# Kernel optimization log

Hardware: AMD Instinct MI355X
Metric: run time of the kernel (lower is better)

The kernel has to match this reference:

```python
import jax, jax.numpy as jnp
import numpy as np

VOCAB = 50000
D = 256          # vector_dim == hidden size
SEQ = 128
BATCH = 4096
NUM_CLASSES = 5


def setup_inputs() -> dict:
    key = jax.random.key(0)
    ks = jax.random.split(key, 8)
    x = jax.random.randint(ks[0], (BATCH, SEQ), 0, VOCAB, dtype=jnp.int64)
    scale = 1.0 / np.sqrt(D)
    emb = jax.random.normal(ks[1], (VOCAB, D), dtype=jnp.float32)
    emb = emb.at[0].set(0.0)  # padding_idx=0 row is zero
    W_ih = jax.random.uniform(ks[2], (D, D), jnp.float32, -scale, scale)
    W_hh = jax.random.uniform(ks[3], (D, D), jnp.float32, -scale, scale)
    b_ih = jax.random.uniform(ks[4], (D,), jnp.float32, -scale, scale)
    b_hh = jax.random.uniform(ks[5], (D,), jnp.float32, -scale, scale)
    W_cls = jax.random.uniform(ks[6], (NUM_CLASSES, D), jnp.float32, -scale, scale)
    b_cls = jax.random.uniform(ks[7], (NUM_CLASSES,), jnp.float32, -scale, scale)
    return {"x": x, "emb": emb, "W_ih": W_ih, "W_hh": W_hh,
            "b_ih": b_ih, "b_hh": b_hh, "W_cls": W_cls, "b_cls": b_cls}


def reference(x, emb, W_ih, W_hh, b_ih, b_hh, W_cls, b_cls):
    # Embedding lookup: [B, S, D]
    xe = emb[x]
    # Precompute input projections for all timesteps in one GEMM.
    x_proj = jnp.einsum("bsd,hd->bsh", xe, W_ih) + b_ih + b_hh  # [B, S, D]

    def step(h, xp_t):
        h = jnp.tanh(xp_t + h @ W_hh.T)
        return h, None

    h0 = jnp.zeros((x.shape[0], W_hh.shape[0]), dtype=xe.dtype)
    # scan over time axis: [S, B, D]
    h_last, _ = jax.lax.scan(step, h0, jnp.swapaxes(x_proj, 0, 1))
    # classifier on last step
    return h_last @ W_cls.T + b_cls  # [B, 5]
```

## Files before the change

kernel.cpp:

```cpp
#include <hip/hip_runtime.h>


typedef __attribute__((ext_vector_type(8))) short bf16x8;
typedef __attribute__((ext_vector_type(4))) float f32x4;

#define VOCAB 50000
#define NBLK_EMB 256
#define LDS_STRIDE 264

__device__ __align__(256) unsigned short g_P[VOCAB * 256];

static __device__ __forceinline__ float bf2f(unsigned short u) {
    union { unsigned int i; float f; } v; v.i = ((unsigned int)u) << 16; return v.f;
}
static __device__ __forceinline__ float bfbits2f(unsigned int zext_u16) {
    union { unsigned int i; float f; } v; v.i = zext_u16 << 16; return v.f;
}
static __device__ __forceinline__ unsigned short f2bf_rne(float f) {
    union { float f; unsigned int i; } v; v.f = f;
    unsigned int r = v.i + 0x7FFFu + ((v.i >> 16) & 1u);
    return (unsigned short)(r >> 16);
}
static __device__ __forceinline__ unsigned short f2bf_fast(float f) {
    union { float f; unsigned int i; } v; v.f = f;
    return (unsigned short)((v.i + 0x8000u) >> 16);
}
static __device__ __forceinline__ bf16x8 cvt8(float4 a, float4 b) {
    bf16x8 r;
    r[0] = (short)f2bf_rne(a.x); r[1] = (short)f2bf_rne(a.y);
    r[2] = (short)f2bf_rne(a.z); r[3] = (short)f2bf_rne(a.w);
    r[4] = (short)f2bf_rne(b.x); r[5] = (short)f2bf_rne(b.y);
    r[6] = (short)f2bf_rne(b.z); r[7] = (short)f2bf_rne(b.w);
    return r;
}
static __device__ __forceinline__ bf16x8 load8_bf(const float* __restrict__ p) {
    return cvt8(((const float4*)p)[0], ((const float4*)p)[1]);
}
static __device__ __forceinline__ float fast_tanh(float x) {
    x = __builtin_amdgcn_fmed3f(x, -8.f, 8.f);
    float e = __expf(2.f * x);
    return __builtin_fmaf(-2.f, __builtin_amdgcn_rcpf(e + 1.f), 1.f);
}

__global__ __launch_bounds__(256)
void emb_proj_kernel(const float* __restrict__ emb,
                     const float* __restrict__ W_ih,
                     const float* __restrict__ b_ih,
                     const float* __restrict__ b_hh)
{
    __shared__ __align__(16) unsigned short tin [16 * LDS_STRIDE];
    __shared__ __align__(16) unsigned short tout[16 * LDS_STRIDE];
    const int tid  = threadIdx.x;
    const int lane = tid & 63;
    const int wid  = tid >> 6;
    const int n0   = wid * 64;
    const int row  = tid >> 4, seg = tid & 15;

    bf16x8 wf[4][8];
    float  bias[4];
    #pragma unroll
    for (int nt = 0; nt < 4; ++nt) {
        int n = n0 + nt * 16 + (lane & 15);
        bias[nt] = b_ih[n] + b_hh[n];
        #pragma unroll
        for (int kt = 0; kt < 8; ++kt)
            wf[nt][kt] = load8_bf(W_ih + n * 256 + (lane >> 4) * 8 + kt * 32);
    }

    int tile = blockIdx.x;
    float4 a0, a1, a2, a3;
    {
        const float4* s = (const float4*)(emb + ((size_t)tile * 16 + row) * 256 + seg * 16);
        a0 = s[0]; a1 = s[1]; a2 = s[2]; a3 = s[3];
    }

    for (; tile < 3125; tile += NBLK_EMB) {
        *(bf16x8*)(&tin[row * LDS_STRIDE + seg * 16])     = cvt8(a0, a1);
        *(bf16x8*)(&tin[row * LDS_STRIDE + seg * 16 + 8]) = cvt8(a2, a3);
        int tn = tile + NBLK_EMB;
        if (tn < 3125) {
            const float4* s = (const float4*)(emb + ((size_t)tn * 16 + row) * 256 + seg * 16);
            a0 = s[0]; a1 = s[1]; a2 = s[2]; a3 = s[3];
        }
        __syncthreads();

        f32x4 acc[4];
        #pragma unroll
        for (int nt = 0; nt < 4; ++nt) acc[nt] = (f32x4){0.f, 0.f, 0.f, 0.f};
        #pragma unroll
        for (int kt = 0; kt < 8; ++kt) {
            bf16x8 a = *(bf16x8*)(&tin[(lane & 15) * LDS_STRIDE + (lane >> 4) * 8 + kt * 32]);
            #pragma unroll
            for (int nt = 0; nt < 4; ++nt)
                acc[nt] = __builtin_amdgcn_mfma_f32_16x16x32_bf16(a, wf[nt][kt], acc[nt], 0, 0, 0);
        }
        #pragma unroll
        for (int nt = 0; nt < 4; ++nt) {
            int n = n0 + nt * 16 + (lane & 15);
            #pragma unroll
            for (int r = 0; r < 4; ++r)
                tout[((lane >> 4) * 4 + r) * LDS_STRIDE + n] = f2bf_rne(acc[nt][r] + bias[nt]);
        }
        __syncthreads();
        {
            uint4 o0 = *(uint4*)(&tout[row * LDS_STRIDE + seg * 16]);
            uint4 o1 = *(uint4*)(&tout[row * LDS_STRIDE + seg * 16 + 8]);
            uint4* dst = (uint4*)(g_P + ((size_t)tile * 16 + row) * 256 + seg * 16);
            dst[0] = o0; dst[1] = o1;
        }
    }
}

__global__ __launch_bounds__(512, 2)
void rnn_kernel(const int* __restrict__ x,
                const float* __restrict__ W_hh,
                const float* __restrict__ W_cls,
                const float* __restrict__ b_cls,
                float* __restrict__ out)
{
    __shared__ __align__(16) unsigned short h_lds[2][16 * 256];
    __shared__ __align__(16) int tok_t[128 * 16];
    __shared__ __align__(16) float wcls_lds[5 * 256];
    __shared__ float bcls_lds[5];

    const int tid  = threadIdx.x;
    const int lane = tid & 63;
    const int wid  = tid >> 6;
    const int b0   = blockIdx.x * 16;
    const int n0   = wid * 32;
    const int l15  = lane & 15;
    const int quad = lane >> 4;

    bf16x8 wf[2][8];
    #pragma unroll
    for (int nt = 0; nt < 2; ++nt) {
        int n = n0 + nt * 16 + l15;
        #pragma unroll
        for (int kt = 0; kt < 8; ++kt)
            wf[nt][kt] = load8_bf(W_hh + n * 256 + quad * 8 + kt * 32);
    }

    {
        int row = tid & 15, tq = tid >> 4;
        int4 v = *(const int4*)(x + (size_t)(b0 + row) * 128 + tq * 4);
        tok_t[(tq * 4 + 0) * 16 + row] = v.x;
        tok_t[(tq * 4 + 1) * 16 + row] = v.y;
        tok_t[(tq * 4 + 2) * 16 + row] = v.z;
        tok_t[(tq * 4 + 3) * 16 + row] = v.w;
    }
    if (tid < 320) ((float4*)wcls_lds)[tid] = ((const float4*)W_cls)[tid];
    if (tid < 5)   bcls_lds[tid] = b_cls[tid];
    #pragma unroll
    for (int i = 0; i < 4; ++i) ((unsigned int*)h_lds[0])[tid + i * 512] = 0;

    int aoff[8];
    #pragma unroll
    for (int kt = 0; kt < 8; ++kt)
        aoff[kt] = l15 * 512 + (((quad + 4 * kt) ^ l15) << 4);
    int woff[8];
    #pragma unroll
    for (int nt = 0; nt < 2; ++nt)
        #pragma unroll
        for (int r = 0; r < 4; ++r) {
            int row = quad * 4 + r;
            int g   = (n0 >> 3) + nt * 2 + (l15 >> 3);
            woff[nt * 4 + r] = row * 512 + ((g ^ row) << 4) + (l15 & 7) * 2;
        }

    const unsigned int colByte = (unsigned int)(n0 + l15) * 2;

    unsigned int gA[8], gB[8];
    #pragma unroll
    for (int r = 0; r < 4; ++r) {
        const int* xr = x + (size_t)(b0 + quad * 4 + r) * 128;
        const unsigned short* p0 = g_P + (size_t)xr[0] * 256 + n0 + l15;
        const unsigned short* p1 = g_P + (size_t)xr[1] * 256 + n0 + l15;
        gA[r] = p0[0]; gA[4 + r] = p0[16];
        gB[r] = p1[0]; gB[4 + r] = p1[16];
    }
    __syncthreads();

    char* const h0 = (char*)&h_lds[0][0];

    auto step = [&](const char* hA, char* hW, unsigned int* g, int t) {
        f32x4 acc0 = { bfbits2f(g[0]), bfbits2f(g[1]), bfbits2f(g[2]), bfbits2f(g[3]) };
        f32x4 acc1 = { bfbits2f(g[4]), bfbits2f(g[5]), bfbits2f(g[6]), bfbits2f(g[7]) };
        if (t + 2 < 128) {
            int4 tk = *(const int4*)&tok_t[(t + 2) * 16 + quad * 4];
            const unsigned short* r0 = (const unsigned short*)((const char*)g_P + ((unsigned int)tk.x * 512 + colByte));
            const unsigned short* r1 = (const unsigned short*)((const char*)g_P + ((unsigned int)tk.y * 512 + colByte));
            const unsigned short* r2 = (const unsigned short*)((const char*)g_P + ((unsigned int)tk.z * 512 + colByte));
            const unsigned short* r3 = (const unsigned short*)((const char*)g_P + ((unsigned int)tk.w * 512 + colByte));
            g[0] = r0[0]; g[4] = r0[16];
            g[1] = r1[0]; g[5] = r1[16];
            g[2] = r2[0]; g[6] = r2[16];
            g[3] = r3[0]; g[7] = r3[16];
        }
        #pragma unroll
        for (int kt = 0; kt < 8; ++kt) {
            bf16x8 a = *(const bf16x8*)(hA + aoff[kt]);
            acc0 = __builtin_amdgcn_mfma_f32_16x16x32_bf16(a, wf[0][kt], acc0, 0, 0, 0);
            acc1 = __builtin_amdgcn_mfma_f32_16x16x32_bf16(a, wf[1][kt], acc1, 0, 0, 0);
        }
        #pragma unroll
        for (int r = 0; r < 4; ++r) {
            *(unsigned short*)(hW + woff[r])     = f2bf_fast(fast_tanh(acc0[r]));
            *(unsigned short*)(hW + woff[4 + r]) = f2bf_fast(fast_tanh(acc1[r]));
        }
    };

    #pragma unroll 1
    for (int t2 = 0; t2 < 64; ++t2) {
        step(h0,        h0 + 8192, gA, 2 * t2);
        __syncthreads();
        step(h0 + 8192, h0,        gB, 2 * t2 + 1);
        __syncthreads();
    }

    if (tid < 320) {
        int q = tid & 3, p = tid >> 2;
        int row = p / 5, c = p - row * 5;
        float acc = 0.f;
        #pragma unroll
        for (int kk = 0; kk < 64; ++kk) {
            int k = q * 64 + kk;
            int off = row * 512 + ((((k >> 3) ^ row)) << 4) + (k & 7) * 2;
            acc += bf2f(*(const unsigned short*)(h0 + off)) * wcls_lds[c * 256 + k];
        }
        acc += __shfl_xor(acc, 1);
        acc += __shfl_xor(acc, 2);
        if (q == 0) out[(size_t)(b0 + row) * 5 + c] = acc + bcls_lds[c];
    }
}

extern "C" void kernel_launch(void* const* d_in, const int* in_sizes, int n_in,
                              void* d_out, int out_size, void* d_ws, size_t ws_size,
                              hipStream_t stream)
{
    const int*   x     = (const int*)d_in[0];
    const float* emb   = (const float*)d_in[1];
    const float* W_ih  = (const float*)d_in[2];
    const float* W_hh  = (const float*)d_in[3];
    const float* b_ih  = (const float*)d_in[4];
    const float* b_hh  = (const float*)d_in[5];
    const float* W_cls = (const float*)d_in[6];
    const float* b_cls = (const float*)d_in[7];
    float*       out   = (float*)d_out;
    (void)d_ws; (void)ws_size;

    emb_proj_kernel<<<NBLK_EMB, 256, 0, stream>>>(emb, W_ih, b_ih, b_hh);
    rnn_kernel<<<256, 512, 0, stream>>>(x, W_hh, W_cls, b_cls, out);
}
```

Baseline: 229.6 us.

## Drop LDS staging in embedding projection and use LDS-only barriers in RNN loop

The embedding projection kernel now loads each wave's A fragments straight from global memory into registers and writes results straight to the global table. This removes the LDS staging buffers and both block barriers per tile, and the grid size and occupancy hint are doubled. In the recurrent kernel, __syncthreads is replaced with a barrier that waits only on LDS/scalar counters, so in-flight global gathers of the next step's projections no longer stall each step's barrier. The risks are uncoalesced 2-byte global stores, redundant A loads across the four waves, and relying on the custom barrier being a correct memory fence for the h_lds exchange.

```diff
diff --git a/kernel.cpp b/kernel.cpp
--- a/kernel.cpp
+++ b/kernel.cpp
@@ -5,8 +5,7 @@
 typedef __attribute__((ext_vector_type(4))) float f32x4;
 
 #define VOCAB 50000
-#define NBLK_EMB 256
-#define LDS_STRIDE 264
+#define NBLK_EMB 512
 
 __device__ __align__(256) unsigned short g_P[VOCAB * 256];
 
@@ -41,72 +40,57 @@
     float e = __expf(2.f * x);
     return __builtin_fmaf(-2.f, __builtin_amdgcn_rcpf(e + 1.f), 1.f);
 }
-
-__global__ __launch_bounds__(256)
+static __device__ __forceinline__ void barrier_lds_only() {
+    asm volatile("s_waitcnt lgkmcnt(0)\n\ts_barrier" ::: "memory");
+}
+
+__global__ __launch_bounds__(256, 2)
 void emb_proj_kernel(const float* __restrict__ emb,
                      const float* __restrict__ W_ih,
                      const float* __restrict__ b_ih,
                      const float* __restrict__ b_hh)
 {
-    __shared__ __align__(16) unsigned short tin [16 * LDS_STRIDE];
-    __shared__ __align__(16) unsigned short tout[16 * LDS_STRIDE];
     const int tid  = threadIdx.x;
     const int lane = tid & 63;
     const int wid  = tid >> 6;
     const int n0   = wid * 64;
-    const int row  = tid >> 4, seg = tid & 15;
+    const int l15  = lane & 15;
+    const int quad = lane >> 4;
 
     bf16x8 wf[4][8];
     float  bias[4];
     #pragma unroll
     for (int nt = 0; nt < 4; ++nt) {
-        int n = n0 + nt * 16 + (lane & 15);
+        int n = n0 + nt * 16 + l15;
         bias[nt] = b_ih[n] + b_hh[n];
         #pragma unroll
         for (int kt = 0; kt < 8; ++kt)
-            wf[nt][kt] = load8_bf(W_ih + n * 256 + (lane >> 4) * 8 + kt * 32);
-    }
-
-    int tile = blockIdx.x;
-    float4 a0, a1, a2, a3;
-    {
-        const float4* s = (const float4*)(emb + ((size_t)tile * 16 + row) * 256 + seg * 16);
-        a0 = s[0]; a1 = s[1]; a2 = s[2]; a3 = s[3];
-    }
-
-    for (; tile < 3125; tile += NBLK_EMB) {
-        *(bf16x8*)(&tin[row * LDS_STRIDE + seg * 16])     = cvt8(a0, a1);
-        *(bf16x8*)(&tin[row * LDS_STRIDE + seg * 16 + 8]) = cvt8(a2, a3);
-        int tn = tile + NBLK_EMB;
-        if (tn < 3125) {
-            const float4* s = (const float4*)(emb + ((size_t)tn * 16 + row) * 256 + seg * 16);
-            a0 = s[0]; a1 = s[1]; a2 = s[2]; a3 = s[3];
-        }
-        __syncthreads();
+            wf[nt][kt] = load8_bf(W_ih + n * 256 + quad * 8 + kt * 32);
+    }
+
+    for (int tile = blockIdx.x; tile < 3125; tile += NBLK_EMB) {
+        const float* arow = emb + ((size_t)tile * 16 + l15) * 256 + quad * 8;
+        bf16x8 a[8];
+        #pragma unroll
+        for (int kt = 0; kt < 8; ++kt)
+            a[kt] = load8_bf(arow + kt * 32);
 
         f32x4 acc[4];
         #pragma unroll
         for (int nt = 0; nt < 4; ++nt) acc[nt] = (f32x4){0.f, 0.f, 0.f, 0.f};
         #pragma unroll
         for (int kt = 0; kt < 8; ++kt) {
-            bf16x8 a = *(bf16x8*)(&tin[(lane & 15) * LDS_STRIDE + (lane >> 4) * 8 + kt * 32]);
             #pragma unroll
             for (int nt = 0; nt < 4; ++nt)
-                acc[nt] = __builtin_amdgcn_mfma_f32_16x16x32_bf16(a, wf[nt][kt], acc[nt], 0, 0, 0);
-        }
+                acc[nt] = __builtin_amdgcn_mfma_f32_16x16x32_bf16(a[kt], wf[nt][kt], acc[nt], 0, 0, 0);
+        }
+
+        unsigned short* prow = g_P + ((size_t)tile * 16 + quad * 4) * 256 + n0;
         #pragma unroll
         for (int nt = 0; nt < 4; ++nt) {
-            int n = n0 + nt * 16 + (lane & 15);
             #pragma unroll
             for (int r = 0; r < 4; ++r)
-                tout[((lane >> 4) * 4 + r) * LDS_STRIDE + n] = f2bf_rne(acc[nt][r] + bias[nt]);
-        }
-        __syncthreads();
-        {
-            uint4 o0 = *(uint4*)(&tout[row * LDS_STRIDE + seg * 16]);
-            uint4 o1 = *(uint4*)(&tout[row * LDS_STRIDE + seg * 16 + 8]);
-            uint4* dst = (uint4*)(g_P + ((size_t)tile * 16 + row) * 256 + seg * 16);
-            dst[0] = o0; dst[1] = o1;
+                prow[r * 256 + nt * 16 + l15] = f2bf_rne(acc[nt][r] + bias[nt]);
         }
     }
 }
@@ -178,7 +162,7 @@
         gA[r] = p0[0]; gA[4 + r] = p0[16];
         gB[r] = p1[0]; gB[4 + r] = p1[16];
     }
-    __syncthreads();
+    barrier_lds_only();
 
     char* const h0 = (char*)&h_lds[0][0];
 
@@ -212,9 +196,9 @@
     #pragma unroll 1
     for (int t2 = 0; t2 < 64; ++t2) {
         step(h0,        h0 + 8192, gA, 2 * t2);
-        __syncthreads();
+        barrier_lds_only();
         step(h0 + 8192, h0,        gB, 2 * t2 + 1);
-        __syncthreads();
+        barrier_lds_only();
     }
 
     if (tid < 320) {
```

Result: slower. 258.8 us (+12.7%).

## Halve RNN block to 4 waves with 64 columns each; lighter barriers

Applied to the files above, without the earlier changes.

The recurrent kernel now runs 256 threads per block, and each wave owns 64 hidden columns (four MFMA N-tiles) instead of 32. This halves the number of waves that meet at each per-timestep barrier and gives each wave more independent MFMAs, at the cost of more registers per wave and fewer waves per CU. Barriers are replaced by a raw s_waitcnt lgkmcnt(0) + s_barrier, so outstanding global gathers no longer stall the barrier. The embedding-projection kernel also gets twice as many blocks and a 2-blocks-per-CU launch bound.

```diff
diff --git a/kernel.cpp b/kernel.cpp
--- a/kernel.cpp
+++ b/kernel.cpp
@@ -5,7 +5,7 @@
 typedef __attribute__((ext_vector_type(4))) float f32x4;
 
 #define VOCAB 50000
-#define NBLK_EMB 256
+#define NBLK_EMB 512
 #define LDS_STRIDE 264
 
 __device__ __align__(256) unsigned short g_P[VOCAB * 256];
@@ -41,8 +41,11 @@
     float e = __expf(2.f * x);
     return __builtin_fmaf(-2.f, __builtin_amdgcn_rcpf(e + 1.f), 1.f);
 }
-
-__global__ __launch_bounds__(256)
+static __device__ __forceinline__ void barrier_lds_only() {
+    asm volatile("s_waitcnt lgkmcnt(0)\n\ts_barrier" ::: "memory");
+}
+
+__global__ __launch_bounds__(256, 2)
 void emb_proj_kernel(const float* __restrict__ emb,
                      const float* __restrict__ W_ih,
                      const float* __restrict__ b_ih,
@@ -82,7 +85,7 @@
             const float4* s = (const float4*)(emb + ((size_t)tn * 16 + row) * 256 + seg * 16);
             a0 = s[0]; a1 = s[1]; a2 = s[2]; a3 = s[3];
         }
-        __syncthreads();
+        barrier_lds_only();
 
         f32x4 acc[4];
         #pragma unroll
@@ -101,7 +104,7 @@
             for (int r = 0; r < 4; ++r)
                 tout[((lane >> 4) * 4 + r) * LDS_STRIDE + n] = f2bf_rne(acc[nt][r] + bias[nt]);
         }
-        __syncthreads();
+        barrier_lds_only();
         {
             uint4 o0 = *(uint4*)(&tout[row * LDS_STRIDE + seg * 16]);
             uint4 o1 = *(uint4*)(&tout[row * LDS_STRIDE + seg * 16 + 8]);
@@ -111,7 +114,7 @@
     }
 }
 
-__global__ __launch_bounds__(512, 2)
+__global__ __launch_bounds__(256, 1)
 void rnn_kernel(const int* __restrict__ x,
                 const float* __restrict__ W_hh,
                 const float* __restrict__ W_cls,
@@ -127,13 +130,13 @@
     const int lane = tid & 63;
     const int wid  = tid >> 6;
     const int b0   = blockIdx.x * 16;
-    const int n0   = wid * 32;
+    const int n0   = wid * 64;
     const int l15  = lane & 15;
     const int quad = lane >> 4;
 
-    bf16x8 wf[2][8];
-    #pragma unroll
-    for (int nt = 0; nt < 2; ++nt) {
+    bf16x8 wf[4][8];
+    #pragma unroll
+    for (int nt = 0; nt < 4; ++nt) {
         int n = n0 + nt * 16 + l15;
         #pragma unroll
         for (int kt = 0; kt < 8; ++kt)
@@ -142,24 +145,29 @@
 
     {
         int row = tid & 15, tq = tid >> 4;
-        int4 v = *(const int4*)(x + (size_t)(b0 + row) * 128 + tq * 4);
-        tok_t[(tq * 4 + 0) * 16 + row] = v.x;
-        tok_t[(tq * 4 + 1) * 16 + row] = v.y;
-        tok_t[(tq * 4 + 2) * 16 + row] = v.z;
-        tok_t[(tq * 4 + 3) * 16 + row] = v.w;
-    }
-    if (tid < 320) ((float4*)wcls_lds)[tid] = ((const float4*)W_cls)[tid];
-    if (tid < 5)   bcls_lds[tid] = b_cls[tid];
-    #pragma unroll
-    for (int i = 0; i < 4; ++i) ((unsigned int*)h_lds[0])[tid + i * 512] = 0;
+        int4 v0 = *(const int4*)(x + (size_t)(b0 + row) * 128 + tq * 8);
+        int4 v1 = *(const int4*)(x + (size_t)(b0 + row) * 128 + tq * 8 + 4);
+        tok_t[(tq * 8 + 0) * 16 + row] = v0.x;
+        tok_t[(tq * 8 + 1) * 16 + row] = v0.y;
+        tok_t[(tq * 8 + 2) * 16 + row] = v0.z;
+        tok_t[(tq * 8 + 3) * 16 + row] = v0.w;
+        tok_t[(tq * 8 + 4) * 16 + row] = v1.x;
+        tok_t[(tq * 8 + 5) * 16 + row] = v1.y;
+        tok_t[(tq * 8 + 6) * 16 + row] = v1.z;
+        tok_t[(tq * 8 + 7) * 16 + row] = v1.w;
+    }
+    for (int i = tid; i < 320; i += 256) ((float4*)wcls_lds)[i] = ((const float4*)W_cls)[i];
+    if (tid < 5) bcls_lds[tid] = b_cls[tid];
+    #pragma unroll
+    for (int i = 0; i < 8; ++i) ((unsigned int*)h_lds[0])[tid + i * 256] = 0;
 
     int aoff[8];
     #pragma unroll
     for (int kt = 0; kt < 8; ++kt)
         aoff[kt] = l15 * 512 + (((quad + 4 * kt) ^ l15) << 4);
-    int woff[8];
-    #pragma unroll
-    for (int nt = 0; nt < 2; ++nt)
+    int woff[16];
+    #pragma unroll
+    for (int nt = 0; nt < 4; ++nt)
         #pragma unroll
         for (int r = 0; r < 4; ++r) {
             int row = quad * 4 + r;
@@ -169,66 +177,75 @@
 
     const unsigned int colByte = (unsigned int)(n0 + l15) * 2;
 
-    unsigned int gA[8], gB[8];
+    unsigned int gA[16], gB[16];
     #pragma unroll
     for (int r = 0; r < 4; ++r) {
         const int* xr = x + (size_t)(b0 + quad * 4 + r) * 128;
         const unsigned short* p0 = g_P + (size_t)xr[0] * 256 + n0 + l15;
         const unsigned short* p1 = g_P + (size_t)xr[1] * 256 + n0 + l15;
-        gA[r] = p0[0]; gA[4 + r] = p0[16];
-        gB[r] = p1[0]; gB[4 + r] = p1[16];
-    }
-    __syncthreads();
+        #pragma unroll
+        for (int nt = 0; nt < 4; ++nt) {
+            gA[nt * 4 + r] = p0[nt * 16];
+            gB[nt * 4 + r] = p1[nt * 16];
+        }
+    }
+    barrier_lds_only();
 
     char* const h0 = (char*)&h_lds[0][0];
 
     auto step = [&](const char* hA, char* hW, unsigned int* g, int t) {
-        f32x4 acc0 = { bfbits2f(g[0]), bfbits2f(g[1]), bfbits2f(g[2]), bfbits2f(g[3]) };
-        f32x4 acc1 = { bfbits2f(g[4]), bfbits2f(g[5]), bfbits2f(g[6]), bfbits2f(g[7]) };
+        f32x4 acc[4];
+        #pragma unroll
+        for (int nt = 0; nt < 4; ++nt)
+            acc[nt] = (f32x4){ bfbits2f(g[nt*4+0]), bfbits2f(g[nt*4+1]),
+                               bfbits2f(g[nt*4+2]), bfbits2f(g[nt*4+3]) };
         if (t + 2 < 128) {
             int4 tk = *(const int4*)&tok_t[(t + 2) * 16 + quad * 4];
-            const unsigned short* r0 = (const unsigned short*)((const char*)g_P + ((unsigned int)tk.x * 512 + colByte));
-            const unsigned short* r1 = (const unsigned short*)((const char*)g_P + ((unsigned int)tk.y * 512 + colByte));
-            const unsigned short* r2 = (const unsigned short*)((const char*)g_P + ((unsigned int)tk.z * 512 + colByte));
-            const unsigned short* r3 = (const unsigned short*)((const char*)g_P + ((unsigned int)tk.w * 512 + colByte));
-            g[0] = r0[0]; g[4] = r0[16];
-            g[1] = r1[0]; g[5] = r1[16];
-            g[2] = r2[0]; g[6] = r2[16];
-            g[3] = r3[0]; g[7] = r3[16];
+            const char* r0 = (const char*)g_P + ((unsigned int)tk.x * 512 + colByte);
+            const char* r1 = (const char*)g_P + ((unsigned int)tk.y * 512 + colByte);
+            const char* r2 = (const char*)g_P + ((unsigned int)tk.z * 512 + colByte);
+            const char* r3 = (const char*)g_P + ((unsigned int)tk.w * 512 + colByte);
+            #pragma unroll
+            for (int nt = 0; nt < 4; ++nt) {
+                g[nt*4+0] = *(const unsigned short*)(r0 + nt * 32);
+                g[nt*4+1] = *(const unsigned short*)(r1 + nt * 32);
+                g[nt*4+2] = *(const unsigned short*)(r2 + nt * 32);
+                g[nt*4+3] = *(const unsigned short*)(r3 + nt * 32);
+            }
         }
         #pragma unroll
         for (int kt = 0; kt < 8; ++kt) {
             bf16x8 a = *(const bf16x8*)(hA + aoff[kt]);
-            acc0 = __builtin_amdgcn_mfma_f32_16x16x32_bf16(a, wf[0][kt], acc0, 0, 0, 0);
-            acc1 = __builtin_amdgcn_mfma_f32_16x16x32_bf16(a, wf[1][kt], acc1, 0, 0, 0);
-        }
-        #pragma unroll
-        for (int r = 0; r < 4; ++r) {
-            *(unsigned short*)(hW + woff[r])     = f2bf_fast(fast_tanh(acc0[r]));
-            *(unsigned short*)(hW + woff[4 + r]) = f2bf_fast(fast_tanh(acc1[r]));
-        }
+            #pragma unroll
+            for (int nt = 0; nt < 4; ++nt)
+                acc[nt] = __builtin_amdgcn_mfma_f32_16x16x32_bf16(a, wf[nt][kt], acc[nt], 0, 0, 0);
+        }
+        #pragma unroll
+        for (int nt = 0; nt < 4; ++nt)
+            #pragma unroll
+            for (int r = 0; r < 4; ++r)
+                *(unsigned short*)(hW + woff[nt*4+r]) = f2bf_fast(fast_tanh(acc[nt][r]));
     };
 
     #pragma unroll 1
     for (int t2 = 0; t2 < 64; ++t2) {
         step(h0,        h0 + 8192, gA, 2 * t2);
-        __syncthreads();
+        barrier_lds_only();
         step(h0 + 8192, h0,        gB, 2 * t2 + 1);
-        __syncthreads();
-    }
-
-    if (tid < 320) {
-        int q = tid & 3, p = tid >> 2;
+        barrier_lds_only();
+    }
+
+    if (tid < 160) {
+        int q = tid & 1, p = tid >> 1;
         int row = p / 5, c = p - row * 5;
         float acc = 0.f;
         #pragma unroll
-        for (int kk = 0; kk < 64; ++kk) {
-            int k = q * 64 + kk;
+        for (int kk = 0; kk < 128; ++kk) {
+            int k = q * 128 + kk;
             int off = row * 512 + ((((k >> 3) ^ row)) << 4) + (k & 7) * 2;
             acc += bf2f(*(const unsigned short*)(h0 + off)) * wcls_lds[c * 256 + k];
         }
         acc += __shfl_xor(acc, 1);
-        acc += __shfl_xor(acc, 2);
         if (q == 0) out[(size_t)(b0 + row) * 5 + c] = acc + bcls_lds[c];
     }
 }
@@ -249,5 +266,5 @@
     (void)d_ws; (void)ws_size;
 
     emb_proj_kernel<<<NBLK_EMB, 256, 0, stream>>>(emb, W_ih, b_ih, b_hh);
-    rnn_kernel<<<256, 512, 0, stream>>>(x, W_hh, W_cls, b_cls, out);
-}
+    rnn_kernel<<<256, 256, 0, stream>>>(x, W_hh, W_cls, b_cls, out);
+}
```

Result: slower. 251.5 us (+9.6%).
